# Kernel optimization log

Measured on AMD Instinct MI355X. Metric: run time of the kernel, lower is better.

## Reference

```python
import jax, jax.numpy as jnp
import numpy as np

MIN_TIMESCALE = 1.0
MAX_TIMESCALE = 10000.0


def llama_rope(x):
    # x: [B, S, N, H]; LLaMA-style interleaved rotary embedding (pairs along last dim).
    B, S, N, H = x.shape
    half = H // 2
    fraction = 2.0 * jnp.arange(0, half, dtype=jnp.float32) / H
    timescale = MIN_TIMESCALE * (MAX_TIMESCALE / MIN_TIMESCALE) ** fraction  # [half]
    position = jnp.arange(S, dtype=jnp.float32)[None, :, None, None]  # [1,S,1,1]
    sinusoid = position / timescale[None, None, None, :]  # [1,S,1,half]
    sin, cos = jnp.sin(sinusoid), jnp.cos(sinusoid)
    xr = x.astype(jnp.float32).reshape(B, S, N, half, 2)
    x1, x2 = xr[..., 0], xr[..., 1]
    r1 = x1 * cos - x2 * sin
    r2 = x2 * cos + x1 * sin
    out = jnp.stack((r1, r2), axis=-1).reshape(B, S, N, H)
    return out.astype(x.dtype)


def setup_inputs() -> dict:
    key = jax.random.key(0)
    kx, kq, kk, kv, ko = jax.random.split(key, 5)
    B, S, D, N, H = 4, 2048, 2048, 16, 128
    x = jax.random.normal(kx, (B, S, D), dtype=jnp.float32)
    # fan_in-style scaling for projection kernels
    wq = jax.random.normal(kq, (D, N, H), dtype=jnp.float32) / np.sqrt(D)
    wk = jax.random.normal(kk, (D, N, H), dtype=jnp.float32) / np.sqrt(D)
    wv = jax.random.normal(kv, (D, N, H), dtype=jnp.float32) / np.sqrt(D)
    wo = jax.random.normal(ko, (N, H, D), dtype=jnp.float32) / np.sqrt(N * H)
    return {"x": x, "wq": wq, "wk": wk, "wv": wv, "wo": wo}


def reference(x, wq, wk, wv, wo):
    # QKV projections (DenseGeneral with features=(num_heads, head_dim))
    q = jnp.einsum("bsd,dnh->bsnh", x, wq)
    k = jnp.einsum("bsd,dnh->bsnh", x, wk)
    v = jnp.einsum("bsd,dnh->bsnh", x, wv)
    # Fused RoPE on query and key (LLaMA interleaved variant)
    q = llama_rope(q)
    k = llama_rope(k)
    head_dim = q.shape[-1]
    q = q / jnp.sqrt(jnp.asarray(head_dim, q.dtype))
    # Causal flash attention (math equivalent: masked softmax attention)
    S = q.shape[1]
    logits = jnp.einsum("bqnh,bknh->bnqk", q, k)  # [B,N,S,S]
    causal = jnp.tril(jnp.ones((S, S), dtype=bool))
    logits = jnp.where(causal[None, None, :, :], logits, jnp.asarray(-1e30, logits.dtype))
    probs = jax.nn.softmax(logits.astype(jnp.float32), axis=-1).astype(v.dtype)
    attn = jnp.einsum("bnqk,bknh->bqnh", probs, v)  # [B,S,N,H]
    # Output projection (DenseGeneral over axes (-2,-1))
    return jnp.einsum("bqnh,nhd->bqd", attn, wo)
```

## Files before the change

### kernel.cpp

```cpp
#include <hip/hip_runtime.h>
#include <hip/hip_bf16.h>
#include <cmath>

#define S_LEN 2048
#define DDIM  2048
#define NHEAD 16
#define HDIM  128
#define BATCH 4
#define KPAD  136
#define VPAD  40
#define PPAD  40

typedef __bf16 bf16;
typedef __attribute__((ext_vector_type(8))) __bf16 bf16x8;
typedef __attribute__((ext_vector_type(4))) __bf16 bf16x4;
typedef __attribute__((ext_vector_type(4))) float  f32x4;

__device__ __forceinline__ void gl_lds(const bf16* g, bf16* l) {
  __builtin_amdgcn_global_load_lds((const __attribute__((address_space(1))) unsigned*)g,
                                   (__attribute__((address_space(3))) unsigned*)l, 16, 0, 0);
}

__global__ __launch_bounds__(256)
void conv_kernel(const float* __restrict__ x, bf16* __restrict__ y) {
  size_t i = ((size_t)blockIdx.x * 256 + threadIdx.x) * 8;
  float4 a = *(const float4*)&x[i];
  float4 b = *(const float4*)&x[i + 4];
  bf16x8 o;
  o[0] = (bf16)a.x; o[1] = (bf16)a.y; o[2] = (bf16)a.z; o[3] = (bf16)a.w;
  o[4] = (bf16)b.x; o[5] = (bf16)b.y; o[6] = (bf16)b.z; o[7] = (bf16)b.w;
  *(bf16x8*)&y[i] = o;
}

__global__ __launch_bounds__(256)
void twconv_kernel(const float* __restrict__ W, bf16* __restrict__ Wt) {
  __shared__ bf16 tile[64][72];
  const int t  = threadIdx.x;
  const int k0 = blockIdx.x * 64;
  const int n0 = blockIdx.y * 64;
#pragma unroll
  for (int it = 0; it < 4; it++) {
    int k = (t >> 4) + it * 16;
    int n = (t & 15) * 4;
    float4 v = *(const float4*)&W[(size_t)(k0 + k) * DDIM + n0 + n];
    tile[k][n + 0] = (bf16)v.x; tile[k][n + 1] = (bf16)v.y;
    tile[k][n + 2] = (bf16)v.z; tile[k][n + 3] = (bf16)v.w;
  }
  __syncthreads();
#pragma unroll
  for (int it = 0; it < 2; it++) {
    int n  = (t >> 3) + it * 32;
    int kc = (t & 7) * 8;
    bf16x8 o;
#pragma unroll
    for (int j = 0; j < 8; j++) o[j] = tile[kc + j][n];
    *(bf16x8*)&Wt[(size_t)(n0 + n) * DDIM + k0 + kc] = o;
  }
}

template <int MODE>
__global__ __launch_bounds__(256)
void gemm_kernel(const bf16* __restrict__ A, const bf16* __restrict__ Bt,
                 void* __restrict__ Out) {
  __shared__ bf16 As[128 * 64];
  __shared__ bf16 Bs[128 * 64];

  const int t    = threadIdx.x;
  const int m0   = blockIdx.y * 128;
  const int n0   = blockIdx.x * 128;
  const int lane = t & 63;
  const int wave = t >> 6;
  const int quad = lane >> 4;
  const int lm   = lane & 15;
  const int wm   = wave >> 1;
  const int wn   = wave & 1;

  f32x4 acc[4][4];
#pragma unroll
  for (int i = 0; i < 4; i++)
#pragma unroll
    for (int j = 0; j < 4; j++) acc[i][j] = (f32x4){0.f, 0.f, 0.f, 0.f};

  const int lrow   = lane >> 3;
  const int lslot  = lane & 7;
  const int lchunk = lslot ^ lrow;
  const int sw     = lm & 7;

  for (int k0 = 0; k0 < DDIM; k0 += 64) {
    __syncthreads();
#pragma unroll
    for (int q = 0; q < 4; q++) {
      const int G   = (wave * 4 + q) * 8;
      const int row = G + lrow;
      gl_lds(&A [(size_t)(m0 + row) * DDIM + k0 + lchunk * 8], &As[G * 64]);
      gl_lds(&Bt[(size_t)(n0 + row) * DDIM + k0 + lchunk * 8], &Bs[G * 64]);
    }
    __syncthreads();

    bf16x8 af[4][2], bfr[4][2];
#pragma unroll
    for (int i = 0; i < 4; i++)
#pragma unroll
      for (int c = 0; c < 2; c++)
        af[i][c] = *(const bf16x8*)&As[(wm * 64 + i * 16 + lm) * 64 + 8 * ((4 * c + quad) ^ sw)];
#pragma unroll
    for (int j = 0; j < 4; j++)
#pragma unroll
      for (int c = 0; c < 2; c++)
        bfr[j][c] = *(const bf16x8*)&Bs[(wn * 64 + j * 16 + lm) * 64 + 8 * ((4 * c + quad) ^ sw)];
#pragma unroll
    for (int c = 0; c < 2; c++)
#pragma unroll
      for (int i = 0; i < 4; i++)
#pragma unroll
        for (int j = 0; j < 4; j++)
          acc[i][j] = __builtin_amdgcn_mfma_f32_16x16x32_bf16(af[i][c], bfr[j][c], acc[i][j], 0, 0, 0);
  }

  const int row_base = m0 + wm * 64;
  const int col_base = n0 + wn * 64;

  if constexpr (MODE == 3) {
    float* O = (float*)Out;
#pragma unroll
    for (int i = 0; i < 4; i++)
#pragma unroll
      for (int j = 0; j < 4; j++)
#pragma unroll
        for (int r = 0; r < 4; r++) {
          int row = row_base + i * 16 + quad * 4 + r;
          int col = col_base + j * 16 + lm;
          O[(size_t)row * DDIM + col] = acc[i][j][r];
        }
  } else if constexpr (MODE == 2) {
    bf16* O = (bf16*)Out;
#pragma unroll
    for (int i = 0; i < 4; i++) {
      int row = row_base + i * 16 + quad * 4;
      int b = row >> 11, s = row & (S_LEN - 1);
#pragma unroll
      for (int j = 0; j < 4; j++) {
        int col = col_base + j * 16 + lm;
        int head = col >> 7, h = col & (HDIM - 1);
        bf16x4 pk;
#pragma unroll
        for (int r = 0; r < 4; r++) pk[r] = (bf16)acc[i][j][r];
        *(bf16x4*)&O[((size_t)(b * NHEAD + head) * HDIM + h) * S_LEN + s] = pk;
      }
    }
  } else {
    bf16* O = (bf16*)Out;
#pragma unroll
    for (int i = 0; i < 4; i++)
#pragma unroll
      for (int j = 0; j < 4; j++)
#pragma unroll
        for (int r = 0; r < 4; r++) {
          int row = row_base + i * 16 + quad * 4 + r;
          int col = col_base + j * 16 + lm;
          int b = row >> 11, s = row & (S_LEN - 1);
          int head = col >> 7, h = col & (HDIM - 1);
          float v = acc[i][j][r];
          float partner = __shfl_xor(v, 1, 64);
          float inv_ts = __expf((float)(h >> 1) * -0.14391156831f);
          float ang = (float)s * inv_ts;
          float sn, cs;
          __sincosf(ang, &sn, &cs);
          float o = ((h & 1) == 0) ? (v * cs - partner * sn) : (v * cs + partner * sn);
          if (MODE == 0) o *= 0.08838834764831845f;
          O[((size_t)(b * NHEAD + head) * S_LEN + s) * HDIM + h] = (bf16)o;
        }
  }
}

__global__ __launch_bounds__(256, 2)
void attn_kernel(const bf16* __restrict__ Q, const bf16* __restrict__ K,
                 const bf16* __restrict__ Vt, bf16* __restrict__ Aout) {
  __shared__ bf16 Ks[32 * KPAD];
  __shared__ bf16 Vs[128 * VPAD];
  __shared__ bf16 Pl[4][32 * PPAD];
  const int t    = threadIdx.x;
  const int lane = t & 63;
  const int wave = t >> 6;
  const int quad = lane >> 4;
  const int lm   = lane & 15;
  const int a    = blockIdx.x;
  const int bh   = blockIdx.y;
  const int lobase = a * 64 + wave * 16;
  const int hibase = 2048 - a * 64 - 64 + wave * 16;
  const size_t hb = (size_t)bh * S_LEN * HDIM;
  const bf16* Qh = Q + hb;
  const bf16* Kh = K + hb;
  const bf16* Vh = Vt + hb;
  bf16* P = &Pl[wave][0];

  bf16x8 qflo[4], qfhi[4];
#pragma unroll
  for (int c = 0; c < 4; c++) {
    qflo[c] = *(const bf16x8*)&Qh[(size_t)(lobase + lm) * HDIM + c * 32 + quad * 8];
    qfhi[c] = *(const bf16x8*)&Qh[(size_t)(hibase + lm) * HDIM + c * 32 + quad * 8];
  }

  bf16 onev = (bf16)1.0f;
  bf16x8 ones = {onev, onev, onev, onev, onev, onev, onev, onev};

  f32x4 olo[8], ohi[8];
#pragma unroll
  for (int hc = 0; hc < 8; hc++) {
    olo[hc] = (f32x4){0.f, 0.f, 0.f, 0.f};
    ohi[hc] = (f32x4){0.f, 0.f, 0.f, 0.f};
  }
  f32x4 llo = (f32x4){0.f, 0.f, 0.f, 0.f};
  f32x4 lhi = (f32x4){0.f, 0.f, 0.f, 0.f};

  const int nkt = 64 - 2 * a;
  const int nlo = 2 * a + (wave >> 1) + 1;
  const int nhi = 63 - 2 * a + (wave >> 1);

  const int c0    = t * 2;
  const int krow0 = c0 >> 4, kcol0 = (c0 & 15) * 8;
  const int vrow0 = c0 >> 2, vcol0 = (c0 & 3) * 8;

  for (int kt = 0; kt < nkt; kt++) {
    const int kb = kt * 32;
    __syncthreads();
    {
      const bf16* kg = &Kh[(size_t)(kb + krow0) * HDIM + kcol0];
      *(bf16x8*)&Ks[krow0 * KPAD + kcol0]     = *(const bf16x8*)kg;
      *(bf16x8*)&Ks[krow0 * KPAD + kcol0 + 8] = *(const bf16x8*)(kg + 8);
      const bf16* vg = &Vh[(size_t)vrow0 * S_LEN + kb + vcol0];
      *(bf16x8*)&Vs[vrow0 * VPAD + vcol0]     = *(const bf16x8*)vg;
      *(bf16x8*)&Vs[vrow0 * VPAD + vcol0 + 8] = *(const bf16x8*)(vg + 8);
    }
    __syncthreads();

    const bool hi_act = kt < nhi;
    const bool lo_act = kt < nlo;

    bf16x8 af[2][4];
#pragma unroll
    for (int cb = 0; cb < 2; cb++)
#pragma unroll
      for (int c = 0; c < 4; c++)
        af[cb][c] = *(const bf16x8*)&Ks[(cb * 16 + lm) * KPAD + c * 32 + quad * 8];

    if (hi_act) {
      f32x4 s[2] = {(f32x4){0.f, 0.f, 0.f, 0.f}, (f32x4){0.f, 0.f, 0.f, 0.f}};
#pragma unroll
      for (int c = 0; c < 4; c++)
#pragma unroll
        for (int cb = 0; cb < 2; cb++)
          s[cb] = __builtin_amdgcn_mfma_f32_16x16x32_bf16(af[cb][c], qfhi[c], s[cb], 0, 0, 0);
#pragma unroll
      for (int cb = 0; cb < 2; cb++) {
        bf16x4 pk;
#pragma unroll
        for (int r = 0; r < 4; r++) {
          int key = kb + cb * 16 + quad * 4 + r;
          float sv = (key <= hibase + lm) ? s[cb][r] : -3.0e38f;
          pk[r] = (bf16)__expf(sv - 12.0f);
        }
        *(bf16x4*)&P[(16 + lm) * PPAD + cb * 16 + quad * 4] = pk;
      }
    }
    if (lo_act) {
      f32x4 s[2] = {(f32x4){0.f, 0.f, 0.f, 0.f}, (f32x4){0.f, 0.f, 0.f, 0.f}};
#pragma unroll
      for (int c = 0; c < 4; c++)
#pragma unroll
        for (int cb = 0; cb < 2; cb++)
          s[cb] = __builtin_amdgcn_mfma_f32_16x16x32_bf16(af[cb][c], qflo[c], s[cb], 0, 0, 0);
#pragma unroll
      for (int cb = 0; cb < 2; cb++) {
        bf16x4 pk;
#pragma unroll
        for (int r = 0; r < 4; r++) {
          int key = kb + cb * 16 + quad * 4 + r;
          float sv = (key <= lobase + lm) ? s[cb][r] : -3.0e38f;
          pk[r] = (bf16)__expf(sv - 12.0f);
        }
        *(bf16x4*)&P[lm * PPAD + cb * 16 + quad * 4] = pk;
      }
    }
    __builtin_amdgcn_s_waitcnt(0xC07F);

    bf16x8 vf[8];
#pragma unroll
    for (int hc = 0; hc < 8; hc++)
      vf[hc] = *(const bf16x8*)&Vs[(hc * 16 + lm) * VPAD + quad * 8];

    if (hi_act) {
      bf16x8 pf = *(const bf16x8*)&P[(16 + lm) * PPAD + quad * 8];
#pragma unroll
      for (int hc = 0; hc < 8; hc++)
        ohi[hc] = __builtin_amdgcn_mfma_f32_16x16x32_bf16(pf, vf[hc], ohi[hc], 0, 0, 0);
      lhi = __builtin_amdgcn_mfma_f32_16x16x32_bf16(pf, ones, lhi, 0, 0, 0);
    }
    if (lo_act) {
      bf16x8 pf = *(const bf16x8*)&P[lm * PPAD + quad * 8];
#pragma unroll
      for (int hc = 0; hc < 8; hc++)
        olo[hc] = __builtin_amdgcn_mfma_f32_16x16x32_bf16(pf, vf[hc], olo[hc], 0, 0, 0);
      llo = __builtin_amdgcn_mfma_f32_16x16x32_bf16(pf, ones, llo, 0, 0, 0);
    }
  }

  const int b = bh >> 4, n = bh & 15;
#pragma unroll
  for (int r = 0; r < 4; r++) {
    float invl = 1.0f / llo[r];
    float invh = 1.0f / lhi[r];
    int ql = lobase + quad * 4 + r;
    int qh = hibase + quad * 4 + r;
    size_t bl = ((size_t)(b * S_LEN + ql) * NHEAD + n) * HDIM;
    size_t bhh = ((size_t)(b * S_LEN + qh) * NHEAD + n) * HDIM;
#pragma unroll
    for (int hc = 0; hc < 8; hc++) {
      Aout[bl  + hc * 16 + lm] = (bf16)(olo[hc][r] * invl);
      Aout[bhh + hc * 16 + lm] = (bf16)(ohi[hc][r] * invh);
    }
  }
}

extern "C" void kernel_launch(void* const* d_in, const int* in_sizes, int n_in,
                              void* d_out, int out_size, void* d_ws, size_t ws_size,
                              hipStream_t stream) {
  const float* x  = (const float*)d_in[0];
  const float* wq = (const float*)d_in[1];
  const float* wk = (const float*)d_in[2];
  const float* wv = (const float*)d_in[3];
  const float* wo = (const float*)d_in[4];
  float* out = (float*)d_out;

  const size_t SZ  = (size_t)BATCH * S_LEN * NHEAD * HDIM;
  const size_t WSZ = (size_t)DDIM * DDIM;
  bf16* Qb = (bf16*)d_ws;
  bf16* Kb = Qb + SZ;
  bf16* Vb = Kb + SZ;
  bf16* Eb = Vb + SZ;

  bf16* WTq = (bf16*)d_out;
  bf16* WTk = WTq + WSZ;
  bf16* WTv = WTk + WSZ;
  bf16* WTo = (bf16*)Qb;

  dim3 blk(256);
  conv_kernel<<<SZ / (256 * 8), blk, 0, stream>>>(x, Eb);
  dim3 gt(32, 32);
  twconv_kernel<<<gt, blk, 0, stream>>>(wq, WTq);
  twconv_kernel<<<gt, blk, 0, stream>>>(wk, WTk);
  twconv_kernel<<<gt, blk, 0, stream>>>(wv, WTv);

  dim3 gg(16, 64);
  gemm_kernel<0><<<gg, blk, 0, stream>>>(Eb, WTq, (void*)Qb);
  gemm_kernel<1><<<gg, blk, 0, stream>>>(Eb, WTk, (void*)Kb);
  gemm_kernel<2><<<gg, blk, 0, stream>>>(Eb, WTv, (void*)Vb);

  dim3 ga(16, BATCH * NHEAD);
  attn_kernel<<<ga, blk, 0, stream>>>(Qb, Kb, Vb, Eb);

  twconv_kernel<<<gt, blk, 0, stream>>>(wo, WTo);
  gemm_kernel<3><<<gg, blk, 0, stream>>>(Eb, WTo, (void*)out);
}
```

Baseline: 672.7 us.

## Enlarge GEMM tiles to 256x256 with double-buffered LDS prefetch

The projection GEMMs move from 128x128 tiles with 4 waves to 256x256 tiles with 8 waves per block. Global-to-LDS loads are double-buffered so the next K-slice is fetched while MFMAs run, using manual waitcnt, barriers and setprio around the MFMA groups. This cuts global traffic per flop and hides load latency, at the cost of 128KB of LDS per block, more accumulator registers and fewer blocks in the grid (256 per GEMM). KPAD in the attention kernel also changes from 136 to 152.

```diff
diff --git a/kernel.cpp b/kernel.cpp
--- a/kernel.cpp
+++ b/kernel.cpp
@@ -7,7 +7,7 @@
 #define NHEAD 16
 #define HDIM  128
 #define BATCH 4
-#define KPAD  136
+#define KPAD  152
 #define VPAD  40
 #define PPAD  40
 
@@ -59,84 +59,144 @@
 }
 
 template <int MODE>
-__global__ __launch_bounds__(256)
+__global__ __launch_bounds__(512, 2)
 void gemm_kernel(const bf16* __restrict__ A, const bf16* __restrict__ Bt,
                  void* __restrict__ Out) {
-  __shared__ bf16 As[128 * 64];
-  __shared__ bf16 Bs[128 * 64];
+  __shared__ bf16 As[2][256 * 64];
+  __shared__ bf16 Bs[2][256 * 64];
 
   const int t    = threadIdx.x;
-  const int m0   = blockIdx.y * 128;
-  const int n0   = blockIdx.x * 128;
+  const int m0   = blockIdx.y * 256;
+  const int n0   = blockIdx.x * 256;
   const int lane = t & 63;
   const int wave = t >> 6;
+  const int wm   = wave >> 2;
+  const int wn   = wave & 3;
   const int quad = lane >> 4;
   const int lm   = lane & 15;
-  const int wm   = wave >> 1;
-  const int wn   = wave & 1;
-
-  f32x4 acc[4][4];
-#pragma unroll
-  for (int i = 0; i < 4; i++)
-#pragma unroll
-    for (int j = 0; j < 4; j++) acc[i][j] = (f32x4){0.f, 0.f, 0.f, 0.f};
+  const int sw   = lm & 7;
 
   const int lrow   = lane >> 3;
   const int lslot  = lane & 7;
   const int lchunk = lslot ^ lrow;
-  const int sw     = lm & 7;
-
-  for (int k0 = 0; k0 < DDIM; k0 += 64) {
-    __syncthreads();
+
+  const int rA = wm * 128 + wn * 32;
+  const int rB = (wn >> 1) * 128 + (wm * 2 + (wn & 1)) * 32;
+  const bf16* gA = &A [(size_t)(m0 + rA + lrow) * DDIM + lchunk * 8];
+  const bf16* gB = &Bt[(size_t)(n0 + rB + lrow) * DDIM + lchunk * 8];
+
+  f32x4 acc[8][4];
+#pragma unroll
+  for (int i = 0; i < 8; i++)
+#pragma unroll
+    for (int j = 0; j < 4; j++) acc[i][j] = (f32x4){0.f, 0.f, 0.f, 0.f};
+
+  auto stage = [&](int k0, int b) {
 #pragma unroll
     for (int q = 0; q < 4; q++) {
-      const int G   = (wave * 4 + q) * 8;
-      const int row = G + lrow;
-      gl_lds(&A [(size_t)(m0 + row) * DDIM + k0 + lchunk * 8], &As[G * 64]);
-      gl_lds(&Bt[(size_t)(n0 + row) * DDIM + k0 + lchunk * 8], &Bs[G * 64]);
-    }
-    __syncthreads();
-
-    bf16x8 af[4][2], bfr[4][2];
-#pragma unroll
-    for (int i = 0; i < 4; i++)
-#pragma unroll
-      for (int c = 0; c < 2; c++)
-        af[i][c] = *(const bf16x8*)&As[(wm * 64 + i * 16 + lm) * 64 + 8 * ((4 * c + quad) ^ sw)];
+      gl_lds(gA + (size_t)q * 8 * DDIM + k0, &As[b][(rA + q * 8) * 64]);
+      gl_lds(gB + (size_t)q * 8 * DDIM + k0, &Bs[b][(rB + q * 8) * 64]);
+    }
+  };
+
+  stage(0, 0);
+  stage(64, 1);
+  asm volatile("s_waitcnt vmcnt(8)" ::: "memory");
+  __builtin_amdgcn_s_barrier();
+
+  const int NT = DDIM / 64;
+#pragma unroll 2
+  for (int tt = 0; tt < NT; ++tt) {
+    const bf16* as = &As[tt & 1][0];
+    const bf16* bs = &Bs[tt & 1][0];
+    bf16x8 af[4], bfr[4];
+
 #pragma unroll
     for (int j = 0; j < 4; j++)
-#pragma unroll
-      for (int c = 0; c < 2; c++)
-        bfr[j][c] = *(const bf16x8*)&Bs[(wn * 64 + j * 16 + lm) * 64 + 8 * ((4 * c + quad) ^ sw)];
-#pragma unroll
-    for (int c = 0; c < 2; c++)
-#pragma unroll
-      for (int i = 0; i < 4; i++)
-#pragma unroll
-        for (int j = 0; j < 4; j++)
-          acc[i][j] = __builtin_amdgcn_mfma_f32_16x16x32_bf16(af[i][c], bfr[j][c], acc[i][j], 0, 0, 0);
-  }
-
-  const int row_base = m0 + wm * 64;
+      bfr[j] = *(const bf16x8*)&bs[(wn * 64 + j * 16 + lm) * 64 + 8 * (quad ^ sw)];
+#pragma unroll
+    for (int i = 0; i < 4; i++)
+      af[i] = *(const bf16x8*)&as[(wm * 128 + i * 16 + lm) * 64 + 8 * (quad ^ sw)];
+    __builtin_amdgcn_s_setprio(1);
+#pragma unroll
+    for (int i = 0; i < 4; i++)
+#pragma unroll
+      for (int j = 0; j < 4; j++)
+        acc[i][j] = __builtin_amdgcn_mfma_f32_16x16x32_bf16(af[i], bfr[j], acc[i][j], 0, 0, 0);
+    __builtin_amdgcn_s_setprio(0);
+    __builtin_amdgcn_sched_barrier(0);
+
+#pragma unroll
+    for (int i = 0; i < 4; i++)
+      af[i] = *(const bf16x8*)&as[(wm * 128 + 64 + i * 16 + lm) * 64 + 8 * (quad ^ sw)];
+    __builtin_amdgcn_s_setprio(1);
+#pragma unroll
+    for (int i = 0; i < 4; i++)
+#pragma unroll
+      for (int j = 0; j < 4; j++)
+        acc[4 + i][j] = __builtin_amdgcn_mfma_f32_16x16x32_bf16(af[i], bfr[j], acc[4 + i][j], 0, 0, 0);
+    __builtin_amdgcn_s_setprio(0);
+    __builtin_amdgcn_sched_barrier(0);
+
+#pragma unroll
+    for (int j = 0; j < 4; j++)
+      bfr[j] = *(const bf16x8*)&bs[(wn * 64 + j * 16 + lm) * 64 + 8 * ((4 + quad) ^ sw)];
+#pragma unroll
+    for (int i = 0; i < 4; i++)
+      af[i] = *(const bf16x8*)&as[(wm * 128 + i * 16 + lm) * 64 + 8 * ((4 + quad) ^ sw)];
+    __builtin_amdgcn_s_setprio(1);
+#pragma unroll
+    for (int i = 0; i < 4; i++)
+#pragma unroll
+      for (int j = 0; j < 4; j++)
+        acc[i][j] = __builtin_amdgcn_mfma_f32_16x16x32_bf16(af[i], bfr[j], acc[i][j], 0, 0, 0);
+    __builtin_amdgcn_s_setprio(0);
+    __builtin_amdgcn_sched_barrier(0);
+
+#pragma unroll
+    for (int i = 0; i < 4; i++)
+      af[i] = *(const bf16x8*)&as[(wm * 128 + 64 + i * 16 + lm) * 64 + 8 * ((4 + quad) ^ sw)];
+    __builtin_amdgcn_s_setprio(1);
+#pragma unroll
+    for (int i = 0; i < 4; i++)
+#pragma unroll
+      for (int j = 0; j < 4; j++)
+        acc[4 + i][j] = __builtin_amdgcn_mfma_f32_16x16x32_bf16(af[i], bfr[j], acc[4 + i][j], 0, 0, 0);
+    __builtin_amdgcn_s_setprio(0);
+    __builtin_amdgcn_sched_barrier(0);
+
+    asm volatile("s_waitcnt lgkmcnt(0)" ::: "memory");
+    __builtin_amdgcn_s_barrier();
+    if (tt + 2 < NT) {
+      stage((tt + 2) * 64, tt & 1);
+      asm volatile("s_waitcnt vmcnt(8)" ::: "memory");
+      __builtin_amdgcn_s_barrier();
+    } else if (tt + 1 < NT) {
+      asm volatile("s_waitcnt vmcnt(0)" ::: "memory");
+      __builtin_amdgcn_s_barrier();
+    }
+  }
+
+  const int row_base = m0 + wm * 128;
   const int col_base = n0 + wn * 64;
 
   if constexpr (MODE == 3) {
     float* O = (float*)Out;
 #pragma unroll
-    for (int i = 0; i < 4; i++)
+    for (int m = 0; m < 8; m++)
 #pragma unroll
       for (int j = 0; j < 4; j++)
 #pragma unroll
         for (int r = 0; r < 4; r++) {
-          int row = row_base + i * 16 + quad * 4 + r;
+          int row = row_base + (m >> 2) * 64 + (m & 3) * 16 + quad * 4 + r;
           int col = col_base + j * 16 + lm;
-          O[(size_t)row * DDIM + col] = acc[i][j][r];
+          O[(size_t)row * DDIM + col] = acc[m][j][r];
         }
   } else if constexpr (MODE == 2) {
     bf16* O = (bf16*)Out;
 #pragma unroll
-    for (int i = 0; i < 4; i++) {
-      int row = row_base + i * 16 + quad * 4;
+    for (int m = 0; m < 8; m++) {
+      int row = row_base + (m >> 2) * 64 + (m & 3) * 16 + quad * 4;
       int b = row >> 11, s = row & (S_LEN - 1);
 #pragma unroll
       for (int j = 0; j < 4; j++) {
@@ -144,23 +204,23 @@
         int head = col >> 7, h = col & (HDIM - 1);
         bf16x4 pk;
 #pragma unroll
-        for (int r = 0; r < 4; r++) pk[r] = (bf16)acc[i][j][r];
+        for (int r = 0; r < 4; r++) pk[r] = (bf16)acc[m][j][r];
         *(bf16x4*)&O[((size_t)(b * NHEAD + head) * HDIM + h) * S_LEN + s] = pk;
       }
     }
   } else {
     bf16* O = (bf16*)Out;
 #pragma unroll
-    for (int i = 0; i < 4; i++)
+    for (int m = 0; m < 8; m++)
 #pragma unroll
       for (int j = 0; j < 4; j++)
 #pragma unroll
         for (int r = 0; r < 4; r++) {
-          int row = row_base + i * 16 + quad * 4 + r;
+          int row = row_base + (m >> 2) * 64 + (m & 3) * 16 + quad * 4 + r;
           int col = col_base + j * 16 + lm;
           int b = row >> 11, s = row & (S_LEN - 1);
           int head = col >> 7, h = col & (HDIM - 1);
-          float v = acc[i][j][r];
+          float v = acc[m][j][r];
           float partner = __shfl_xor(v, 1, 64);
           float inv_ts = __expf((float)(h >> 1) * -0.14391156831f);
           float ang = (float)s * inv_ts;
@@ -351,14 +411,15 @@
   twconv_kernel<<<gt, blk, 0, stream>>>(wk, WTk);
   twconv_kernel<<<gt, blk, 0, stream>>>(wv, WTv);
 
-  dim3 gg(16, 64);
-  gemm_kernel<0><<<gg, blk, 0, stream>>>(Eb, WTq, (void*)Qb);
-  gemm_kernel<1><<<gg, blk, 0, stream>>>(Eb, WTk, (void*)Kb);
-  gemm_kernel<2><<<gg, blk, 0, stream>>>(Eb, WTv, (void*)Vb);
+  dim3 blk2(512);
+  dim3 gg(DDIM / 256, (BATCH * S_LEN) / 256);
+  gemm_kernel<0><<<gg, blk2, 0, stream>>>(Eb, WTq, (void*)Qb);
+  gemm_kernel<1><<<gg, blk2, 0, stream>>>(Eb, WTk, (void*)Kb);
+  gemm_kernel<2><<<gg, blk2, 0, stream>>>(Eb, WTv, (void*)Vb);
 
   dim3 ga(16, BATCH * NHEAD);
   attn_kernel<<<ga, blk, 0, stream>>>(Qb, Kb, Vb, Eb);
 
   twconv_kernel<<<gt, blk, 0, stream>>>(wo, WTo);
-  gemm_kernel<3><<<gg, blk, 0, stream>>>(Eb, WTo, (void*)out);
-}
+  gemm_kernel<3><<<gg, blk2, 0, stream>>>(Eb, WTo, (void*)out);
+}
```

Measured after the change: 612.5 us. -8.9%, faster.
